# Optimization experiments

Measured on AMD Instinct MI355X. Metric: run time of the kernel, lower is better.

The kernel has to match this reference:

```python
import jax, jax.numpy as jnp
from jax import lax
import numpy as np

DIM = 512      # latent channel dim
K = 1024       # codebook size
KS = 320       # conv kernel size (== stride -> non-overlapping frames)
STRIDE = 320
B, L = 16, 160000  # 10s of 16kHz audio


def setup_inputs() -> dict:
    key = jax.random.key(0)
    ks = jax.random.split(key, 8)
    wav = jax.random.normal(ks[0], (B, 1, L), jnp.float32)
    enc_w = jax.random.normal(ks[1], (DIM, 1, KS), jnp.float32) * 0.05
    enc_b = jnp.zeros((DIM,), jnp.float32)
    codebook = jax.random.normal(ks[2], (K, DIM), jnp.float32)
    lin_w = jax.random.normal(ks[3], (DIM, DIM), jnp.float32) * 0.02
    lin_b = jnp.zeros((DIM,), jnp.float32)
    film_w = jax.random.normal(ks[4], (2 * DIM, DIM), jnp.float32) * 0.02
    film_b = jnp.zeros((2 * DIM,), jnp.float32)
    dec_w = jax.random.normal(ks[5], (DIM, 1, KS), jnp.float32) * 0.05
    dec_b = jnp.zeros((1,), jnp.float32)
    return dict(wav=wav, enc_w=enc_w, enc_b=enc_b, codebook=codebook,
                lin_w=lin_w, lin_b=lin_b, film_w=film_w, film_b=film_b,
                dec_w=dec_w, dec_b=dec_b)


def reference(wav, enc_w, enc_b, codebook, lin_w, lin_b, film_w, film_b, dec_w, dec_b):
    # --- NAC encoder: strided Conv1d, wav [B,1,L] -> emb [B,D,T] ---
    emb = lax.conv_general_dilated(
        wav, enc_w, window_strides=(STRIDE,), padding='VALID',
        dimension_numbers=('NCH', 'OIH', 'NCH')) + enc_b[None, :, None]

    # --- time-averaged embedding for conditioning ---
    time_avg = emb.mean(axis=-1)  # [B, D]

    # --- VQ encode: nearest codebook entry per frame ---
    x = emb.transpose(0, 2, 1)  # [B, T, D]
    # squared L2 distances [B, T, K]
    dist = (x * x).sum(-1, keepdims=True) \
         - 2.0 * jnp.einsum('btd,kd->btk', x, codebook) \
         + (codebook * codebook).sum(-1)
    codes = jnp.argmin(dist, axis=-1)  # [B, T] int

    # --- VQ decode: codebook gather ---
    emb_r = codebook[codes].transpose(0, 2, 1)  # [B, D, T]

    # --- linear on pooled embedding ---
    cond = time_avg @ lin_w.T + lin_b  # [B, D]

    # --- FiLM modulation: gamma * x + beta per channel ---
    gb = cond @ film_w.T + film_b      # [B, 2D]
    gamma, beta = jnp.split(gb, 2, axis=-1)
    modulated = gamma[:, :, None] * emb_r + beta[:, :, None]  # [B, D, T]

    # --- NAC decoder: transposed Conv1d back to waveform [B,1,L] ---
    out = lax.conv_transpose(
        modulated, dec_w, strides=(STRIDE,), padding='VALID',
        dimension_numbers=('NCH', 'IOH', 'NCH')) + dec_b[None, :, None]
    return out
```

## Files before the change

kernel.cpp:

```cpp
#include <hip/hip_runtime.h>

#define FR   8000
#define FRP  8192
#define DD   512
#define CK   1024
#define KSZ  320
#define TT   500
#define NB   16

typedef unsigned int u32;
typedef unsigned short u16;
typedef __attribute__((ext_vector_type(8))) short b8;
typedef __attribute__((ext_vector_type(4))) float f4;

__device__ __forceinline__ float bf2f(u16 h) {
    u32 u = ((u32)h) << 16;
    return __builtin_bit_cast(float, u);
}
__device__ __forceinline__ u16 f2bf(float f) {
    u32 u = __builtin_bit_cast(u32, f);
    u32 r = u + 0x7FFFu + ((u >> 16) & 1u);
    return (u16)(r >> 16);
}

__device__ __forceinline__ void gld16(const u16* g, u16* s) {
    __builtin_amdgcn_global_load_lds(
        (const __attribute__((address_space(1))) u32*)g,
        (__attribute__((address_space(3))) u32*)s, 16, 0, 0);
}

__device__ __forceinline__ f4 mfma(b8 a, b8 b, f4 c) {
    return __builtin_amdgcn_mfma_f32_16x16x32_bf16(a, b, c, 0, 0, 0);
}

__device__ __forceinline__ void split8(float4 a, float4 b, u16* dh, u16* dl) {
    float xs[8] = {a.x, a.y, a.z, a.w, b.x, b.y, b.z, b.w};
    union { u16 u[8]; b8 v; } H, L;
#pragma unroll
    for (int i = 0; i < 8; ++i) {
        u16 h = f2bf(xs[i]);
        H.u[i] = h;
        L.u[i] = f2bf(xs[i] - bf2f(h));
    }
    *(b8*)dh = H.v;
    *(b8*)dl = L.v;
}

__global__ __launch_bounds__(256) void k_prep(const float* __restrict__ enc_w,
                                              u16* __restrict__ ewh, u16* __restrict__ ewl,
                                              const float* __restrict__ cb,
                                              u16* __restrict__ cbh, u16* __restrict__ cbl,
                                              const float* __restrict__ dw,
                                              u16* __restrict__ dwfh, u16* __restrict__ dwfl,
                                              float* __restrict__ cbn,
                                              const float* __restrict__ wav,
                                              u16* __restrict__ wavh, u16* __restrict__ wavl) {
    const int bid = blockIdx.x, tid = threadIdx.x;
    if (bid < 80) {
        int i = (bid * 256 + tid) * 8;
        float4 a = *(const float4*)&enc_w[i];
        float4 b = *(const float4*)&enc_w[i + 4];
        split8(a, b, &ewh[i], &ewl[i]);
    } else if (bid < 336) {
        int i = ((bid - 80) * 256 + tid) * 8;
        float4 a = *(const float4*)&cb[i];
        float4 b = *(const float4*)&cb[i + 4];
        split8(a, b, &cbh[i], &cbl[i]);
    } else if (bid < 368) {
        int c = (bid - 336) * 32 + (tid >> 3);
        int l = tid & 7;
        float s = 0.f;
        for (int j = l * 4; j < DD; j += 32) {
            float4 v = *(const float4*)&cb[c * DD + j];
            s += v.x * v.x + v.y * v.y + v.z * v.z + v.w * v.w;
        }
        s += __shfl_xor(s, 1);
        s += __shfl_xor(s, 2);
        s += __shfl_xor(s, 4);
        if (l == 0) cbn[c] = s;
    } else if (bid < 1618) {
        int i = ((bid - 368) * 256 + tid) * 8;
        float4 a = *(const float4*)&wav[i];
        float4 b = *(const float4*)&wav[i + 4];
        split8(a, b, &wavh[i], &wavl[i]);
    } else {
        int bid2 = bid - 1618;
        int d0 = (bid2 & 7) * 64;
        int sb = bid2 >> 3;
        int s0 = sb * 64;
        if (sb == 5) {
            b8 z = {};
#pragma unroll
            for (int k = 0; k < 2; ++k) {
                int lin = tid * 2 + k;
                int row = 320 + (lin >> 3);
                int col = (lin & 7) * 8;
                *(b8*)&dwfh[(size_t)row * DD + d0 + col] = z;
                *(b8*)&dwfl[(size_t)row * DD + d0 + col] = z;
            }
            return;
        }
        __shared__ float t64[64][68];
        const int u0 = 256 - s0;
#pragma unroll
        for (int p = 0; p < 4; ++p) {
            int row = (tid >> 4) + 16 * p;
            int c4 = (tid & 15) * 4;
            float4 v = *(const float4*)&dw[(size_t)(d0 + row) * KSZ + u0 + c4];
            t64[row][c4] = v.x; t64[row][c4 + 1] = v.y;
            t64[row][c4 + 2] = v.z; t64[row][c4 + 3] = v.w;
        }
        __syncthreads();
        const int i = tid >> 2;
        const int jq = (tid & 3) * 16;
        union { u16 u[8]; b8 v; } H0, L0, H1, L1;
#pragma unroll
        for (int j = 0; j < 8; ++j) {
            float m = t64[jq + j][63 - i];
            u16 h = f2bf(m);
            H0.u[j] = h; L0.u[j] = f2bf(m - bf2f(h));
            float m2 = t64[jq + 8 + j][63 - i];
            u16 h2 = f2bf(m2);
            H1.u[j] = h2; L1.u[j] = f2bf(m2 - bf2f(h2));
        }
        size_t o = (size_t)(s0 + i) * DD + d0 + jq;
        *(b8*)&dwfh[o] = H0.v; *(b8*)&dwfh[o + 8] = H1.v;
        *(b8*)&dwfl[o] = L0.v; *(b8*)&dwfl[o + 8] = L1.v;
    }
}

#define PIPELINE(NT, STRIDE)                                                  \
    stg(0, 0);                                                                \
    stg(1, STRIDE);                                                           \
    int cur = 0;                                                              \
    for (int t = 0; t < NT; ++t) {                                            \
        if (t < NT - 1) asm volatile("s_waitcnt vmcnt(8)" ::: "memory");      \
        else            asm volatile("s_waitcnt vmcnt(0)" ::: "memory");      \
        __builtin_amdgcn_s_barrier();                                         \
        asm volatile("" ::: "memory");                                        \
        compute(cur);                                                         \
        asm volatile("" ::: "memory");                                        \
        __builtin_amdgcn_s_barrier();                                         \
        if (t < NT - 2) stg(cur, (t + 2) * STRIDE);                           \
        cur ^= 1;                                                             \
    }

__global__ __launch_bounds__(256, 2) void k_enc(const u16* __restrict__ Ahg,
                                                const u16* __restrict__ Alg,
                                                const u16* __restrict__ Bhg,
                                                const u16* __restrict__ Blg,
                                                const float* __restrict__ eb,
                                                u16* __restrict__ embh,
                                                u16* __restrict__ embl) {
    __shared__ __align__(16) u16 Ah[2][4096], Al[2][4096], Bh[2][4096], Bl[2][4096];
    const int tid = threadIdx.x;
    const int l = tid & 63, w = tid >> 6, wm = w >> 1, wn = w & 1;
    const int lane16 = l & 15, laneK = l >> 4;
    const int g = blockIdx.x;
    const int xcd = g & 7, slot = g >> 3;
    const int f0 = (xcd * 8 + (slot & 7)) * 128;
    const int d0 = (slot >> 3) * 128;

    const int p0 = w * 128 + l, p1 = p0 + 64;
    const int r0 = p0 >> 2, q0 = (p0 & 3) ^ ((r0 >> 1) & 3);
    const int r1 = p1 >> 2, q1 = (p1 & 3) ^ ((r1 >> 1) & 3);
    int fa0 = f0 + r0; if (fa0 > FR - 1) fa0 = FR - 1;
    int fa1 = f0 + r1; if (fa1 > FR - 1) fa1 = FR - 1;
    const u16* gA0h = Ahg + (size_t)fa0 * KSZ + q0 * 8;
    const u16* gA1h = Ahg + (size_t)fa1 * KSZ + q1 * 8;
    const u16* gA0l = Alg + (size_t)fa0 * KSZ + q0 * 8;
    const u16* gA1l = Alg + (size_t)fa1 * KSZ + q1 * 8;
    const u16* gB0h = Bhg + (size_t)(d0 + r0) * KSZ + q0 * 8;
    const u16* gB1h = Bhg + (size_t)(d0 + r1) * KSZ + q1 * 8;
    const u16* gB0l = Blg + (size_t)(d0 + r0) * KSZ + q0 * 8;
    const u16* gB1l = Blg + (size_t)(d0 + r1) * KSZ + q1 * 8;

    int offA[4], offB[4];
#pragma unroll
    for (int i = 0; i < 4; ++i) {
        int ra = wm * 64 + i * 16 + lane16;
        offA[i] = (ra * 4 + (laneK ^ ((ra >> 1) & 3))) * 8;
        int rb = wn * 64 + i * 16 + lane16;
        offB[i] = (rb * 4 + (laneK ^ ((rb >> 1) & 3))) * 8;
    }

    f4 zero = {0.f, 0.f, 0.f, 0.f};
    f4 acc[4][4];
#pragma unroll
    for (int i = 0; i < 4; ++i)
#pragma unroll
        for (int j = 0; j < 4; ++j) acc[i][j] = zero;

    auto stg = [&](int buf, int kt) {
        gld16(gA0h + kt, Ah[buf] + w * 1024);
        gld16(gA1h + kt, Ah[buf] + w * 1024 + 512);
        gld16(gA0l + kt, Al[buf] + w * 1024);
        gld16(gA1l + kt, Al[buf] + w * 1024 + 512);
        gld16(gB0h + kt, Bh[buf] + w * 1024);
        gld16(gB1h + kt, Bh[buf] + w * 1024 + 512);
        gld16(gB0l + kt, Bl[buf] + w * 1024);
        gld16(gB1l + kt, Bl[buf] + w * 1024 + 512);
    };
    auto compute = [&](int buf) {
        b8 ah[4], al[4], bh[4], bl[4];
#pragma unroll
        for (int i = 0; i < 4; ++i) {
            ah[i] = *(const b8*)(Ah[buf] + offA[i]);
            al[i] = *(const b8*)(Al[buf] + offA[i]);
            bh[i] = *(const b8*)(Bh[buf] + offB[i]);
            bl[i] = *(const b8*)(Bl[buf] + offB[i]);
        }
#pragma unroll
        for (int mi = 0; mi < 4; ++mi)
#pragma unroll
            for (int ni = 0; ni < 4; ++ni) {
                acc[mi][ni] = mfma(ah[mi], bh[ni], acc[mi][ni]);
                acc[mi][ni] = mfma(ah[mi], bl[ni], acc[mi][ni]);
                acc[mi][ni] = mfma(al[mi], bh[ni], acc[mi][ni]);
            }
    };

    PIPELINE(10, 32)

    float ebv[4];
#pragma unroll
    for (int ni = 0; ni < 4; ++ni) ebv[ni] = eb[d0 + wn * 64 + ni * 16 + lane16];
#pragma unroll
    for (int mi = 0; mi < 4; ++mi)
#pragma unroll
        for (int q = 0; q < 4; ++q) {
            int f = f0 + wm * 64 + mi * 16 + laneK * 4 + q;
#pragma unroll
            for (int ni = 0; ni < 4; ++ni) {
                int d = d0 + wn * 64 + ni * 16 + lane16;
                float v = acc[mi][ni][q] + ebv[ni];
                u16 h = f2bf(v);
                size_t o = (size_t)f * DD + d;
                embh[o] = h;
                embl[o] = f2bf(v - bf2f(h));
            }
        }
}

__global__ __launch_bounds__(256) void k_tavg(const u16* __restrict__ eh,
                                              const u16* __restrict__ el,
                                              float* __restrict__ tavg) {
    const int b = blockIdx.y, d0 = blockIdx.x * 64;
    const int dt = threadIdx.x & 7, tg = threadIdx.x >> 3;
    const int d = d0 + dt * 8;
    float s[8] = {};
    for (int t = tg; t < TT; t += 32) {
        size_t o = (size_t)(b * TT + t) * DD + d;
        b8 h = *(const b8*)(eh + o);
        b8 lo = *(const b8*)(el + o);
#pragma unroll
        for (int j = 0; j < 8; ++j) s[j] += bf2f((u16)h[j]) + bf2f((u16)lo[j]);
    }
#pragma unroll
    for (int m = 8; m <= 32; m <<= 1)
#pragma unroll
        for (int j = 0; j < 8; ++j) s[j] += __shfl_xor(s[j], m);
    __shared__ float red[4][64];
    const int w = threadIdx.x >> 6;
    if ((threadIdx.x & 63) < 8)
#pragma unroll
        for (int j = 0; j < 8; ++j) red[w][dt * 8 + j] = s[j];
    __syncthreads();
    if (threadIdx.x < 64)
        tavg[b * DD + d0 + threadIdx.x] =
            (red[0][threadIdx.x] + red[1][threadIdx.x] +
             red[2][threadIdx.x] + red[3][threadIdx.x]) * (1.0f / TT);
}

__global__ __launch_bounds__(256) void k_cond(const float* __restrict__ tavg,
                                              const float* __restrict__ lw,
                                              const float* __restrict__ lb,
                                              float* __restrict__ cond) {
    __shared__ float stv[NB * DD];
    for (int i = threadIdx.x * 4; i < NB * DD; i += 1024)
        *(float4*)&stv[i] = *(const float4*)&tavg[i];
    __syncthreads();
    const int w = threadIdx.x >> 6, lane = threadIdx.x & 63;
    const int row = blockIdx.x * 4 + w;
    float wv[8];
#pragma unroll
    for (int j = 0; j < 8; ++j) wv[j] = lw[(size_t)row * DD + lane + 64 * j];
    float r[NB];
#pragma unroll
    for (int b = 0; b < NB; ++b) {
        float s = 0.f;
#pragma unroll
        for (int j = 0; j < 8; ++j) s += wv[j] * stv[b * DD + lane + 64 * j];
        r[b] = s;
    }
#pragma unroll
    for (int m = 32; m >= 1; m >>= 1)
#pragma unroll
        for (int b = 0; b < NB; ++b) r[b] += __shfl_xor(r[b], m);
    if (lane < NB) cond[lane * DD + row] = r[lane] + lb[row];
}

__global__ __launch_bounds__(256) void k_film(const float* __restrict__ cond,
                                              const float* __restrict__ fw,
                                              const float* __restrict__ fb,
                                              float* __restrict__ gbv) {
    __shared__ float sc[NB * DD];
    for (int i = threadIdx.x * 4; i < NB * DD; i += 1024)
        *(float4*)&sc[i] = *(const float4*)&cond[i];
    __syncthreads();
    const int w = threadIdx.x >> 6, lane = threadIdx.x & 63;
    const int row = blockIdx.x * 4 + w;
    float wv[8];
#pragma unroll
    for (int j = 0; j < 8; ++j) wv[j] = fw[(size_t)row * DD + lane + 64 * j];
    float r[NB];
#pragma unroll
    for (int b = 0; b < NB; ++b) {
        float s = 0.f;
#pragma unroll
        for (int j = 0; j < 8; ++j) s += wv[j] * sc[b * DD + lane + 64 * j];
        r[b] = s;
    }
#pragma unroll
    for (int m = 32; m >= 1; m >>= 1)
#pragma unroll
        for (int b = 0; b < NB; ++b) r[b] += __shfl_xor(r[b], m);
    if (lane < NB) gbv[lane * 2 * DD + row] = r[lane] + fb[row];
}

__global__ __launch_bounds__(256, 2) void k_dist(const u16* __restrict__ Ahg,
                                                 const u16* __restrict__ Alg,
                                                 const u16* __restrict__ Bhg,
                                                 const u16* __restrict__ Blg,
                                                 const float* __restrict__ cbn,
                                                 float* __restrict__ pmin,
                                                 int* __restrict__ pidx) {
    __shared__ __align__(16) u16 Ah[2][4096], Al[2][4096], Bh[2][4096], Bl[2][4096];
    __shared__ float s_best[128][2];
    __shared__ int s_bidx[128][2];
    const int tid = threadIdx.x;
    const int l = tid & 63, w = tid >> 6, wm = w >> 1, wn = w & 1;
    const int lane16 = l & 15, laneK = l >> 4;
    const int g = blockIdx.x;
    const int xcd = g & 7, slot = g >> 3;
    const int f0 = (xcd * 8 + (slot & 7)) * 128;
    const int cy = slot >> 3;
    const int c0 = cy * 128;

    const int p0 = w * 128 + l, p1 = p0 + 64;
    const int r0 = p0 >> 2, q0 = (p0 & 3) ^ ((r0 >> 1) & 3);
    const int r1 = p1 >> 2, q1 = (p1 & 3) ^ ((r1 >> 1) & 3);
    const u16* gA0h = Ahg + (size_t)(f0 + r0) * DD + q0 * 8;
    const u16* gA1h = Ahg + (size_t)(f0 + r1) * DD + q1 * 8;
    const u16* gA0l = Alg + (size_t)(f0 + r0) * DD + q0 * 8;
    const u16* gA1l = Alg + (size_t)(f0 + r1) * DD + q1 * 8;
    const u16* gB0h = Bhg + (size_t)(c0 + r0) * DD + q0 * 8;
    const u16* gB1h = Bhg + (size_t)(c0 + r1) * DD + q1 * 8;
    const u16* gB0l = Blg + (size_t)(c0 + r0) * DD + q0 * 8;
    const u16* gB1l = Blg + (size_t)(c0 + r1) * DD + q1 * 8;

    int offA[4], offB[4];
#pragma unroll
    for (int i = 0; i < 4; ++i) {
        int ra = wm * 64 + i * 16 + lane16;
        offA[i] = (ra * 4 + (laneK ^ ((ra >> 1) & 3))) * 8;
        int rb = wn * 64 + i * 16 + lane16;
        offB[i] = (rb * 4 + (laneK ^ ((rb >> 1) & 3))) * 8;
    }

    f4 zero = {0.f, 0.f, 0.f, 0.f};
    f4 acc[4][4];
#pragma unroll
    for (int i = 0; i < 4; ++i)
#pragma unroll
        for (int j = 0; j < 4; ++j) acc[i][j] = zero;

    auto stg = [&](int buf, int kt) {
        gld16(gA0h + kt, Ah[buf] + w * 1024);
        gld16(gA1h + kt, Ah[buf] + w * 1024 + 512);
        gld16(gA0l + kt, Al[buf] + w * 1024);
        gld16(gA1l + kt, Al[buf] + w * 1024 + 512);
        gld16(gB0h + kt, Bh[buf] + w * 1024);
        gld16(gB1h + kt, Bh[buf] + w * 1024 + 512);
        gld16(gB0l + kt, Bl[buf] + w * 1024);
        gld16(gB1l + kt, Bl[buf] + w * 1024 + 512);
    };
    auto compute = [&](int buf) {
        b8 ah[4], al[4], bh[4], bl[4];
#pragma unroll
        for (int i = 0; i < 4; ++i) {
            ah[i] = *(const b8*)(Ah[buf] + offA[i]);
            al[i] = *(const b8*)(Al[buf] + offA[i]);
            bh[i] = *(const b8*)(Bh[buf] + offB[i]);
            bl[i] = *(const b8*)(Bl[buf] + offB[i]);
        }
#pragma unroll
        for (int mi = 0; mi < 4; ++mi)
#pragma unroll
            for (int ni = 0; ni < 4; ++ni) {
                acc[mi][ni] = mfma(ah[mi], bh[ni], acc[mi][ni]);
                acc[mi][ni] = mfma(ah[mi], bl[ni], acc[mi][ni]);
                acc[mi][ni] = mfma(al[mi], bh[ni], acc[mi][ni]);
            }
    };

    PIPELINE(16, 32)

    float cbv[4];
    int cidx[4];
#pragma unroll
    for (int ni = 0; ni < 4; ++ni) {
        cidx[ni] = c0 + wn * 64 + ni * 16 + lane16;
        cbv[ni] = cbn[cidx[ni]];
    }
#pragma unroll
    for (int mi = 0; mi < 4; ++mi)
#pragma unroll
        for (int q = 0; q < 4; ++q) {
            float best = 3.4e38f;
            int bi = 0x7fffffff;
#pragma unroll
            for (int ni = 0; ni < 4; ++ni) {
                float s = cbv[ni] - 2.0f * acc[mi][ni][q];
                if (s < best || (s == best && cidx[ni] < bi)) { best = s; bi = cidx[ni]; }
            }
#pragma unroll
            for (int m = 8; m >= 1; m >>= 1) {
                float os = __shfl_xor(best, m);
                int oi = __shfl_xor(bi, m);
                if (os < best || (os == best && oi < bi)) { best = os; bi = oi; }
            }
            if (lane16 == 0) {
                int rl = wm * 64 + mi * 16 + laneK * 4 + q;
                s_best[rl][wn] = best;
                s_bidx[rl][wn] = bi;
            }
        }
    __syncthreads();
    if (tid < 128) {
        float b0 = s_best[tid][0], b1 = s_best[tid][1];
        int i0 = s_bidx[tid][0], i1 = s_bidx[tid][1];
        bool t1 = (b1 < b0) || (b1 == b0 && i1 < i0);
        int f = f0 + tid;
        if (f < FR) {
            pmin[f * 8 + cy] = t1 ? b1 : b0;
            pidx[f * 8 + cy] = t1 ? i1 : i0;
        }
    }
}

__global__ __launch_bounds__(256, 2) void k_dec(const float* __restrict__ pmin,
                                                const int* __restrict__ pidx,
                                                const float* __restrict__ cb,
                                                const float* __restrict__ gbv,
                                                const u16* __restrict__ Bhg,
                                                const u16* __restrict__ Blg,
                                                const float* __restrict__ db,
                                                float* __restrict__ out) {
    __shared__ __align__(16) u16 Ah[2][4096], Al[2][4096], Bh[2][4096], Bl[2][4096];
    __shared__ int codes_lds[128];
    __shared__ int b_lds[128];
    const int tid = threadIdx.x;
    const int l = tid & 63, w = tid >> 6, wm = w >> 1, wn = w & 1;
    const int lane16 = l & 15, laneK = l >> 4;
    const int f0 = blockIdx.y * 128, s0 = blockIdx.x * 128;

    if (tid < 128) {
        int f = f0 + tid;
        int fc = (f < FR) ? f : FR - 1;
        float best = pmin[fc * 8];
        int bi = pidx[fc * 8];
#pragma unroll
        for (int y = 1; y < 8; ++y) {
            float s = pmin[fc * 8 + y];
            if (s < best) { best = s; bi = pidx[fc * 8 + y]; }
        }
        codes_lds[tid] = bi;
        b_lds[tid] = fc / TT;
    }
    __syncthreads();

    const int p0 = w * 128 + l, p1 = p0 + 64;
    const int r0 = p0 >> 2, q0 = (p0 & 3) ^ ((r0 >> 1) & 3);
    const int r1 = p1 >> 2, q1 = (p1 & 3) ^ ((r1 >> 1) & 3);
    const u16* gB0h = Bhg + (size_t)(s0 + r0) * DD + q0 * 8;
    const u16* gB1h = Bhg + (size_t)(s0 + r1) * DD + q1 * 8;
    const u16* gB0l = Blg + (size_t)(s0 + r0) * DD + q0 * 8;
    const u16* gB1l = Blg + (size_t)(s0 + r1) * DD + q1 * 8;

    const int pa0 = tid, pa1 = tid + 256;
    const int ra0 = pa0 >> 2, qa0 = (pa0 & 3) ^ ((ra0 >> 1) & 3);
    const int ra1 = pa1 >> 2, qa1 = (pa1 & 3) ^ ((ra1 >> 1) & 3);
    const float* cp0 = cb + (size_t)codes_lds[ra0] * DD + qa0 * 8;
    const float* cp1 = cb + (size_t)codes_lds[ra1] * DD + qa1 * 8;
    const float* gp0 = gbv + b_lds[ra0] * 2 * DD + qa0 * 8;
    const float* gp1 = gbv + b_lds[ra1] * 2 * DD + qa1 * 8;

    int offA[4], offB[4];
#pragma unroll
    for (int i = 0; i < 4; ++i) {
        int ra = wm * 64 + i * 16 + lane16;
        offA[i] = (ra * 4 + (laneK ^ ((ra >> 1) & 3))) * 8;
        int rb = wn * 64 + i * 16 + lane16;
        offB[i] = (rb * 4 + (laneK ^ ((rb >> 1) & 3))) * 8;
    }

    f4 zero = {0.f, 0.f, 0.f, 0.f};
    f4 acc[4][4];
#pragma unroll
    for (int i = 0; i < 4; ++i)
#pragma unroll
        for (int j = 0; j < 4; ++j) acc[i][j] = zero;

    auto stgB = [&](int buf, int kt) {
        gld16(gB0h + kt, Bh[buf] + w * 1024);
        gld16(gB1h + kt, Bh[buf] + w * 1024 + 512);
        gld16(gB0l + kt, Bl[buf] + w * 1024);
        gld16(gB1l + kt, Bl[buf] + w * 1024 + 512);
    };
    auto stageA = [&](int buf, int kt) {
        float4 c00 = *(const float4*)(cp0 + kt);
        float4 c01 = *(const float4*)(cp0 + kt + 4);
        float4 g00 = *(const float4*)(gp0 + kt);
        float4 g01 = *(const float4*)(gp0 + kt + 4);
        float4 e00 = *(const float4*)(gp0 + DD + kt);
        float4 e01 = *(const float4*)(gp0 + DD + kt + 4);
        float4 c10 = *(const float4*)(cp1 + kt);
        float4 c11 = *(const float4*)(cp1 + kt + 4);
        float4 g10 = *(const float4*)(gp1 + kt);
        float4 g11 = *(const float4*)(gp1 + kt + 4);
        float4 e10 = *(const float4*)(gp1 + DD + kt);
        float4 e11 = *(const float4*)(gp1 + DD + kt + 4);
        float4 m00, m01, m10, m11;
        m00.x = g00.x * c00.x + e00.x; m00.y = g00.y * c00.y + e00.y;
        m00.z = g00.z * c00.z + e00.z; m00.w = g00.w * c00.w + e00.w;
        m01.x = g01.x * c01.x + e01.x; m01.y = g01.y * c01.y + e01.y;
        m01.z = g01.z * c01.z + e01.z; m01.w = g01.w * c01.w + e01.w;
        m10.x = g10.x * c10.x + e10.x; m10.y = g10.y * c10.y + e10.y;
        m10.z = g10.z * c10.z + e10.z; m10.w = g10.w * c10.w + e10.w;
        m11.x = g11.x * c11.x + e11.x; m11.y = g11.y * c11.y + e11.y;
        m11.z = g11.z * c11.z + e11.z; m11.w = g11.w * c11.w + e11.w;
        split8(m00, m01, Ah[buf] + pa0 * 8, Al[buf] + pa0 * 8);
        split8(m10, m11, Ah[buf] + pa1 * 8, Al[buf] + pa1 * 8);
    };
    auto compute = [&](int buf) {
        b8 ah[4], al[4], bh[4], bl[4];
#pragma unroll
        for (int i = 0; i < 4; ++i) {
            ah[i] = *(const b8*)(Ah[buf] + offA[i]);
            al[i] = *(const b8*)(Al[buf] + offA[i]);
            bh[i] = *(const b8*)(Bh[buf] + offB[i]);
            bl[i] = *(const b8*)(Bl[buf] + offB[i]);
        }
#pragma unroll
        for (int mi = 0; mi < 4; ++mi)
#pragma unroll
            for (int ni = 0; ni < 4; ++ni) {
                acc[mi][ni] = mfma(ah[mi], bh[ni], acc[mi][ni]);
                acc[mi][ni] = mfma(ah[mi], bl[ni], acc[mi][ni]);
                acc[mi][ni] = mfma(al[mi], bh[ni], acc[mi][ni]);
            }
    };

    stgB(0, 0); stageA(0, 0);
    stgB(1, 32); stageA(1, 32);
    int cur = 0;
    for (int t = 0; t < 16; ++t) {
        asm volatile("s_waitcnt vmcnt(0) lgkmcnt(0)" ::: "memory");
        __builtin_amdgcn_s_barrier();
        asm volatile("" ::: "memory");
        compute(cur);
        asm volatile("" ::: "memory");
        __builtin_amdgcn_s_barrier();
        if (t < 14) { stgB(cur, (t + 2) * 32); stageA(cur, (t + 2) * 32); }
        cur ^= 1;
    }

    const float d0v = db[0];
#pragma unroll
    for (int mi = 0; mi < 4; ++mi)
#pragma unroll
        for (int q = 0; q < 4; ++q) {
            int f = f0 + wm * 64 + mi * 16 + laneK * 4 + q;
            if (f < FR) {
#pragma unroll
                for (int ni = 0; ni < 4; ++ni) {
                    int s = s0 + wn * 64 + ni * 16 + lane16;
                    if (s < KSZ) out[(size_t)f * KSZ + s] = acc[mi][ni][q] + d0v;
                }
            }
        }
}

extern "C" void kernel_launch(void* const* d_in, const int* in_sizes, int n_in,
                              void* d_out, int out_size, void* d_ws, size_t ws_size,
                              hipStream_t stream) {
    const float* wav    = (const float*)d_in[0];
    const float* enc_w  = (const float*)d_in[1];
    const float* enc_b  = (const float*)d_in[2];
    const float* cb     = (const float*)d_in[3];
    const float* lin_w  = (const float*)d_in[4];
    const float* lin_b  = (const float*)d_in[5];
    const float* film_w = (const float*)d_in[6];
    const float* film_b = (const float*)d_in[7];
    const float* dec_w  = (const float*)d_in[8];
    const float* dec_b  = (const float*)d_in[9];
    float* out = (float*)d_out;

    char* p = (char*)d_ws;
    u16* embh = (u16*)p;                 p += (size_t)FRP * DD * 2;
    u16* embl = (u16*)p;                 p += (size_t)FRP * DD * 2;
    u16* wavh = (u16*)p;                 p += (size_t)FR * KSZ * 2;
    u16* wavl = (u16*)p;                 p += (size_t)FR * KSZ * 2;
    u16* ewh  = (u16*)p;                 p += (size_t)DD * KSZ * 2;
    u16* ewl  = (u16*)p;                 p += (size_t)DD * KSZ * 2;
    u16* cbh  = (u16*)p;                 p += (size_t)CK * DD * 2;
    u16* cbl  = (u16*)p;                 p += (size_t)CK * DD * 2;
    u16* dwfh = (u16*)p;                 p += (size_t)384 * DD * 2;
    u16* dwfl = (u16*)p;                 p += (size_t)384 * DD * 2;
    float* cbn  = (float*)p;             p += CK * 4;
    float* tavg = (float*)p;             p += NB * DD * 4;
    float* cond = (float*)p;             p += NB * DD * 4;
    float* gbv  = (float*)p;             p += NB * 2 * DD * 4;
    float* pmin = (float*)p;             p += FR * 8 * 4;
    int*   pidx = (int*)p;               p += FR * 8 * 4;

    k_prep<<<dim3(1666), 256, 0, stream>>>(enc_w, ewh, ewl, cb, cbh, cbl,
                                           dec_w, dwfh, dwfl, cbn, wav, wavh, wavl);
    k_enc<<<dim3(256), 256, 0, stream>>>(wavh, wavl, ewh, ewl, enc_b, embh, embl);
    k_tavg<<<dim3(8, NB), 256, 0, stream>>>(embh, embl, tavg);
    k_cond<<<dim3(128), 256, 0, stream>>>(tavg, lin_w, lin_b, cond);
    k_film<<<dim3(256), 256, 0, stream>>>(cond, film_w, film_b, gbv);
    k_dist<<<dim3(512), 256, 0, stream>>>(embh, embl, cbh, cbl, cbn, pmin, pidx);
    k_dec<<<dim3(3, 63), 256, 0, stream>>>(pmin, pidx, cb, gbv, dwfh, dwfl, dec_b, out);
}
```

Before: 180.2 us.

## Fuse time-average into encoder epilogue and prefetch decoder A loads earlier

The separate k_tavg kernel is removed. The encoder epilogue now reduces each block's fp32 outputs per batch segment (a 128-frame tile spans at most two batches), and atomically adds the sums into a tsum buffer that an extra k_prep block zeroes. k_cond applies the 1/T scaling. Separately, the decoder's A-operand global loads are issued before the B async loads and the wait is relaxed to vmcnt(4), so global latency can overlap more. This saves one launch and a re-read of emb, at the cost of float atomics (order-dependent summation) and more register pressure in k_dec.

```diff
diff --git a/kernel.cpp b/kernel.cpp
--- a/kernel.cpp
+++ b/kernel.cpp
@@ -54,7 +54,8 @@
                                               u16* __restrict__ dwfh, u16* __restrict__ dwfl,
                                               float* __restrict__ cbn,
                                               const float* __restrict__ wav,
-                                              u16* __restrict__ wavh, u16* __restrict__ wavl) {
+                                              u16* __restrict__ wavh, u16* __restrict__ wavl,
+                                              float* __restrict__ tsum) {
     const int bid = blockIdx.x, tid = threadIdx.x;
     if (bid < 80) {
         int i = (bid * 256 + tid) * 8;
@@ -83,7 +84,7 @@
         float4 a = *(const float4*)&wav[i];
         float4 b = *(const float4*)&wav[i + 4];
         split8(a, b, &wavh[i], &wavl[i]);
-    } else {
+    } else if (bid < 1666) {
         int bid2 = bid - 1618;
         int d0 = (bid2 & 7) * 64;
         int sb = bid2 >> 3;
@@ -126,6 +127,11 @@
         size_t o = (size_t)(s0 + i) * DD + d0 + jq;
         *(b8*)&dwfh[o] = H0.v; *(b8*)&dwfh[o + 8] = H1.v;
         *(b8*)&dwfl[o] = L0.v; *(b8*)&dwfl[o + 8] = L1.v;
+    } else {
+        float4 z = {0.f, 0.f, 0.f, 0.f};
+#pragma unroll
+        for (int k = 0; k < 8; ++k)
+            *(float4*)&tsum[(tid * 8 + k) * 4] = z;
     }
 }
 
@@ -151,8 +157,10 @@
                                                 const u16* __restrict__ Blg,
                                                 const float* __restrict__ eb,
                                                 u16* __restrict__ embh,
-                                                u16* __restrict__ embl) {
+                                                u16* __restrict__ embl,
+                                                float* __restrict__ tsum) {
     __shared__ __align__(16) u16 Ah[2][4096], Al[2][4096], Bh[2][4096], Bl[2][4096];
+    __shared__ float tred[2][128][2];
     const int tid = threadIdx.x;
     const int l = tid & 63, w = tid >> 6, wm = w >> 1, wn = w & 1;
     const int lane16 = l & 15, laneK = l >> 4;
@@ -225,11 +233,17 @@
     float ebv[4];
 #pragma unroll
     for (int ni = 0; ni < 4; ++ni) ebv[ni] = eb[d0 + wn * 64 + ni * 16 + lane16];
+
+    const int bA = f0 / TT;
+    const int fB = min((bA + 1) * TT, f0 + 128);
+    float sumA[4] = {}, sumB[4] = {};
 #pragma unroll
     for (int mi = 0; mi < 4; ++mi)
 #pragma unroll
         for (int q = 0; q < 4; ++q) {
             int f = f0 + wm * 64 + mi * 16 + laneK * 4 + q;
+            bool live = f < FR;
+            bool sideA = f < fB;
 #pragma unroll
             for (int ni = 0; ni < 4; ++ni) {
                 int d = d0 + wn * 64 + ni * 16 + lane16;
@@ -238,47 +252,45 @@
                 size_t o = (size_t)f * DD + d;
                 embh[o] = h;
                 embl[o] = f2bf(v - bf2f(h));
-            }
-        }
-}
-
-__global__ __launch_bounds__(256) void k_tavg(const u16* __restrict__ eh,
-                                              const u16* __restrict__ el,
-                                              float* __restrict__ tavg) {
-    const int b = blockIdx.y, d0 = blockIdx.x * 64;
-    const int dt = threadIdx.x & 7, tg = threadIdx.x >> 3;
-    const int d = d0 + dt * 8;
-    float s[8] = {};
-    for (int t = tg; t < TT; t += 32) {
-        size_t o = (size_t)(b * TT + t) * DD + d;
-        b8 h = *(const b8*)(eh + o);
-        b8 lo = *(const b8*)(el + o);
-#pragma unroll
-        for (int j = 0; j < 8; ++j) s[j] += bf2f((u16)h[j]) + bf2f((u16)lo[j]);
-    }
-#pragma unroll
-    for (int m = 8; m <= 32; m <<= 1)
-#pragma unroll
-        for (int j = 0; j < 8; ++j) s[j] += __shfl_xor(s[j], m);
-    __shared__ float red[4][64];
-    const int w = threadIdx.x >> 6;
-    if ((threadIdx.x & 63) < 8)
-#pragma unroll
-        for (int j = 0; j < 8; ++j) red[w][dt * 8 + j] = s[j];
+                if (live) { if (sideA) sumA[ni] += v; else sumB[ni] += v; }
+            }
+        }
+#pragma unroll
+    for (int m = 16; m <= 32; m <<= 1)
+#pragma unroll
+        for (int ni = 0; ni < 4; ++ni) {
+            sumA[ni] += __shfl_xor(sumA[ni], m);
+            sumB[ni] += __shfl_xor(sumB[ni], m);
+        }
+    if (laneK == 0)
+#pragma unroll
+        for (int ni = 0; ni < 4; ++ni) {
+            tred[wm][wn * 64 + ni * 16 + lane16][0] = sumA[ni];
+            tred[wm][wn * 64 + ni * 16 + lane16][1] = sumB[ni];
+        }
     __syncthreads();
-    if (threadIdx.x < 64)
-        tavg[b * DD + d0 + threadIdx.x] =
-            (red[0][threadIdx.x] + red[1][threadIdx.x] +
-             red[2][threadIdx.x] + red[3][threadIdx.x]) * (1.0f / TT);
-}
-
-__global__ __launch_bounds__(256) void k_cond(const float* __restrict__ tavg,
+    if (tid < 128 && bA < NB) {
+        float a = tred[0][tid][0] + tred[1][tid][0];
+        int d = d0 + tid;
+        atomicAdd(&tsum[bA * DD + d], a);
+        if (fB < f0 + 128 && bA + 1 < NB) {
+            float b = tred[0][tid][1] + tred[1][tid][1];
+            atomicAdd(&tsum[(bA + 1) * DD + d], b);
+        }
+    }
+}
+
+__global__ __launch_bounds__(256) void k_cond(const float* __restrict__ tsum,
                                               const float* __restrict__ lw,
                                               const float* __restrict__ lb,
                                               float* __restrict__ cond) {
     __shared__ float stv[NB * DD];
-    for (int i = threadIdx.x * 4; i < NB * DD; i += 1024)
-        *(float4*)&stv[i] = *(const float4*)&tavg[i];
+    const float inv = 1.0f / TT;
+    for (int i = threadIdx.x * 4; i < NB * DD; i += 1024) {
+        float4 v = *(const float4*)&tsum[i];
+        v.x *= inv; v.y *= inv; v.z *= inv; v.w *= inv;
+        *(float4*)&stv[i] = v;
+    }
     __syncthreads();
     const int w = threadIdx.x >> 6, lane = threadIdx.x & 63;
     const int row = blockIdx.x * 4 + w;
@@ -449,6 +461,11 @@
     }
 }
 
+struct AV {
+    float4 c00, c01, g00, g01, e00, e01;
+    float4 c10, c11, g10, g11, e10, e11;
+};
+
 __global__ __launch_bounds__(256, 2) void k_dec(const float* __restrict__ pmin,
                                                 const int* __restrict__ pidx,
                                                 const float* __restrict__ cb,
@@ -518,28 +535,32 @@
         gld16(gB0l + kt, Bl[buf] + w * 1024);
         gld16(gB1l + kt, Bl[buf] + w * 1024 + 512);
     };
-    auto stageA = [&](int buf, int kt) {
-        float4 c00 = *(const float4*)(cp0 + kt);
-        float4 c01 = *(const float4*)(cp0 + kt + 4);
-        float4 g00 = *(const float4*)(gp0 + kt);
-        float4 g01 = *(const float4*)(gp0 + kt + 4);
-        float4 e00 = *(const float4*)(gp0 + DD + kt);
-        float4 e01 = *(const float4*)(gp0 + DD + kt + 4);
-        float4 c10 = *(const float4*)(cp1 + kt);
-        float4 c11 = *(const float4*)(cp1 + kt + 4);
-        float4 g10 = *(const float4*)(gp1 + kt);
-        float4 g11 = *(const float4*)(gp1 + kt + 4);
-        float4 e10 = *(const float4*)(gp1 + DD + kt);
-        float4 e11 = *(const float4*)(gp1 + DD + kt + 4);
+    auto loadA = [&](int kt) {
+        AV v;
+        v.c00 = *(const float4*)(cp0 + kt);
+        v.c01 = *(const float4*)(cp0 + kt + 4);
+        v.g00 = *(const float4*)(gp0 + kt);
+        v.g01 = *(const float4*)(gp0 + kt + 4);
+        v.e00 = *(const float4*)(gp0 + DD + kt);
+        v.e01 = *(const float4*)(gp0 + DD + kt + 4);
+        v.c10 = *(const float4*)(cp1 + kt);
+        v.c11 = *(const float4*)(cp1 + kt + 4);
+        v.g10 = *(const float4*)(gp1 + kt);
+        v.g11 = *(const float4*)(gp1 + kt + 4);
+        v.e10 = *(const float4*)(gp1 + DD + kt);
+        v.e11 = *(const float4*)(gp1 + DD + kt + 4);
+        return v;
+    };
+    auto writeA = [&](int buf, const AV& v) {
         float4 m00, m01, m10, m11;
-        m00.x = g00.x * c00.x + e00.x; m00.y = g00.y * c00.y + e00.y;
-        m00.z = g00.z * c00.z + e00.z; m00.w = g00.w * c00.w + e00.w;
-        m01.x = g01.x * c01.x + e01.x; m01.y = g01.y * c01.y + e01.y;
-        m01.z = g01.z * c01.z + e01.z; m01.w = g01.w * c01.w + e01.w;
-        m10.x = g10.x * c10.x + e10.x; m10.y = g10.y * c10.y + e10.y;
-        m10.z = g10.z * c10.z + e10.z; m10.w = g10.w * c10.w + e10.w;
-        m11.x = g11.x * c11.x + e11.x; m11.y = g11.y * c11.y + e11.y;
-        m11.z = g11.z * c11.z + e11.z; m11.w = g11.w * c11.w + e11.w;
+        m00.x = v.g00.x * v.c00.x + v.e00.x; m00.y = v.g00.y * v.c00.y + v.e00.y;
+        m00.z = v.g00.z * v.c00.z + v.e00.z; m00.w = v.g00.w * v.c00.w + v.e00.w;
+        m01.x = v.g01.x * v.c01.x + v.e01.x; m01.y = v.g01.y * v.c01.y + v.e01.y;
+        m01.z = v.g01.z * v.c01.z + v.e01.z; m01.w = v.g01.w * v.c01.w + v.e01.w;
+        m10.x = v.g10.x * v.c10.x + v.e10.x; m10.y = v.g10.y * v.c10.y + v.e10.y;
+        m10.z = v.g10.z * v.c10.z + v.e10.z; m10.w = v.g10.w * v.c10.w + v.e10.w;
+        m11.x = v.g11.x * v.c11.x + v.e11.x; m11.y = v.g11.y * v.c11.y + v.e11.y;
+        m11.z = v.g11.z * v.c11.z + v.e11.z; m11.w = v.g11.w * v.c11.w + v.e11.w;
         split8(m00, m01, Ah[buf] + pa0 * 8, Al[buf] + pa0 * 8);
         split8(m10, m11, Ah[buf] + pa1 * 8, Al[buf] + pa1 * 8);
     };
@@ -562,17 +583,28 @@
             }
     };
 
-    stgB(0, 0); stageA(0, 0);
-    stgB(1, 32); stageA(1, 32);
+    {
+        AV v0 = loadA(0);
+        AV v1 = loadA(32);
+        stgB(0, 0);
+        stgB(1, 32);
+        writeA(0, v0);
+        writeA(1, v1);
+    }
     int cur = 0;
     for (int t = 0; t < 16; ++t) {
-        asm volatile("s_waitcnt vmcnt(0) lgkmcnt(0)" ::: "memory");
+        if (t < 15) asm volatile("s_waitcnt vmcnt(4) lgkmcnt(0)" ::: "memory");
+        else        asm volatile("s_waitcnt vmcnt(0) lgkmcnt(0)" ::: "memory");
         __builtin_amdgcn_s_barrier();
         asm volatile("" ::: "memory");
         compute(cur);
         asm volatile("" ::: "memory");
         __builtin_amdgcn_s_barrier();
-        if (t < 14) { stgB(cur, (t + 2) * 32); stageA(cur, (t + 2) * 32); }
+        if (t < 14) {
+            AV v = loadA((t + 2) * 32);
+            stgB(cur, (t + 2) * 32);
+            writeA(cur, v);
+        }
         cur ^= 1;
     }
 
@@ -619,17 +651,16 @@
     u16* dwfh = (u16*)p;                 p += (size_t)384 * DD * 2;
     u16* dwfl = (u16*)p;                 p += (size_t)384 * DD * 2;
     float* cbn  = (float*)p;             p += CK * 4;
-    float* tavg = (float*)p;             p += NB * DD * 4;
+    float* tsum = (float*)p;             p += NB * DD * 4;
     float* cond = (float*)p;             p += NB * DD * 4;
     float* gbv  = (float*)p;             p += NB * 2 * DD * 4;
     float* pmin = (float*)p;             p += FR * 8 * 4;
     int*   pidx = (int*)p;               p += FR * 8 * 4;
 
-    k_prep<<<dim3(1666), 256, 0, stream>>>(enc_w, ewh, ewl, cb, cbh, cbl,
-                                           dec_w, dwfh, dwfl, cbn, wav, wavh, wavl);
-    k_enc<<<dim3(256), 256, 0, stream>>>(wavh, wavl, ewh, ewl, enc_b, embh, embl);
-    k_tavg<<<dim3(8, NB), 256, 0, stream>>>(embh, embl, tavg);
-    k_cond<<<dim3(128), 256, 0, stream>>>(tavg, lin_w, lin_b, cond);
+    k_prep<<<dim3(1667), 256, 0, stream>>>(enc_w, ewh, ewl, cb, cbh, cbl,
+                                           dec_w, dwfh, dwfl, cbn, wav, wavh, wavl, tsum);
+    k_enc<<<dim3(256), 256, 0, stream>>>(wavh, wavl, ewh, ewl, enc_b, embh, embl, tsum);
+    k_cond<<<dim3(128), 256, 0, stream>>>(tsum, lin_w, lin_b, cond);
     k_film<<<dim3(256), 256, 0, stream>>>(cond, film_w, film_b, gbv);
     k_dist<<<dim3(512), 256, 0, stream>>>(embh, embl, cbh, cbl, cbn, pmin, pidx);
     k_dec<<<dim3(3, 63), 256, 0, stream>>>(pmin, pidx, cb, gbv, dwfh, dwfl, dec_b, out);
```

Result: faster. 172.9 us (-4.0%).
